# Kernel optimization log

Hardware: AMD Instinct MI355X
Metric: run time of the kernel (lower is better)

Reference implementation:

```python
import jax, jax.numpy as jnp
import numpy as np
import math

N_HEAD = 16
N_CTX = 1024


def setup_inputs() -> dict:
    key = jax.random.key(0)
    ks = jax.random.split(key, 3)
    B, S, NX = 4, 1024, 1024
    x = jax.random.normal(ks[0], (B, S, NX), dtype=jnp.float32)
    # Conv1D weights stored as [nx, nf], init std=0.02, bias zeros
    c_attn_w = jax.random.normal(ks[1], (NX, 3 * NX), dtype=jnp.float32) * 0.02
    c_attn_b = jnp.zeros((3 * NX,), dtype=jnp.float32)
    c_proj_w = jax.random.normal(ks[2], (NX, NX), dtype=jnp.float32) * 0.02
    c_proj_b = jnp.zeros((NX,), dtype=jnp.float32)
    return {"x": x, "c_attn_w": c_attn_w, "c_attn_b": c_attn_b,
            "c_proj_w": c_proj_w, "c_proj_b": c_proj_b}


def reference(x, c_attn_w, c_attn_b, c_proj_w, c_proj_b):
    B, S, NX = x.shape
    H = N_HEAD
    D = NX // H
    # c_attn: Conv1D -> x @ W + b, then split into q, k, v
    qkv = x @ c_attn_w + c_attn_b                      # [B,S,3*NX]
    q, k, v = jnp.split(qkv, 3, axis=-1)               # each [B,S,NX]
    # split heads: q,v -> [B,H,S,D]; k -> [B,H,D,S]
    q = q.reshape(B, S, H, D).transpose(0, 2, 1, 3)
    k = k.reshape(B, S, H, D).transpose(0, 2, 3, 1)
    v = v.reshape(B, S, H, D).transpose(0, 2, 1, 3)
    # _attn: scores, scale, combined multiplicative+additive causal mask, softmax
    w = jnp.matmul(q, k)                               # [B,H,S,S]
    w = w / math.sqrt(D)                               # scale=True
    bias = jnp.tril(jnp.ones((S, S), dtype=w.dtype))[None, None]  # causal tril slice
    w = w * bias - 1e10 * (1.0 - bias)
    w = jax.nn.softmax(w, axis=-1)
    a = jnp.matmul(w, v)                               # [B,H,S,D]
    # merge heads
    a = a.transpose(0, 2, 1, 3).reshape(B, S, NX)
    # c_proj
    return a @ c_proj_w + c_proj_b
```

## Files before the change

kernel.cpp:

```cpp
#include <hip/hip_runtime.h>
#include <cstdint>

typedef __attribute__((ext_vector_type(8))) short short8;
typedef __attribute__((ext_vector_type(4))) short short4x;
typedef __attribute__((ext_vector_type(4))) float floatx4;

__device__ __forceinline__ unsigned short f2b(float f) {
    unsigned int u = __builtin_bit_cast(unsigned int, f);
    u += 0x7fffu + ((u >> 16) & 1u);
    return (unsigned short)(u >> 16);
}
__device__ __forceinline__ float b2f(unsigned short s) {
    unsigned int u = ((unsigned int)s) << 16;
    return __builtin_bit_cast(float, u);
}
__device__ __forceinline__ float fast_exp2(float x) {
    float r;
    asm("v_exp_f32 %0, %1" : "=v"(r) : "v"(x));
    return r;
}
__device__ __forceinline__ unsigned int pack_bf16_trunc(float lo, float hi) {
    return __builtin_amdgcn_perm(__builtin_bit_cast(unsigned int, hi),
                                 __builtin_bit_cast(unsigned int, lo), 0x07060302u);
}

#define GLDS(g, l) __builtin_amdgcn_global_load_lds(                                   \
    (const __attribute__((address_space(1))) unsigned int*)(g),                        \
    (__attribute__((address_space(3))) unsigned int*)(l), 16, 0, 0)

__global__ __launch_bounds__(256) void prep_kernel(const float* __restrict__ x,
                                                   unsigned short* __restrict__ xb,
                                                   const float* __restrict__ w1,
                                                   unsigned short* __restrict__ w1t,
                                                   const float* __restrict__ w2,
                                                   unsigned short* __restrict__ w2t) {
    __shared__ unsigned short tile[64][65];
    const int b = blockIdx.x, t = threadIdx.x;
    if (b < 1024) {
        for (int i = b * 256 + t; i < 1048576; i += 262144) {
            float4 v = ((const float4*)x)[i];
            ushort4 o;
            o.x = f2b(v.x); o.y = f2b(v.y); o.z = f2b(v.z); o.w = f2b(v.w);
            ((ushort4*)xb)[i] = o;
        }
        return;
    }
    const float* W; unsigned short* Wt; int K, N, kb, nb;
    if (b < 1792) { W = w1; Wt = w1t; K = 1024; N = 3072; kb = (b - 1024) & 15; nb = (b - 1024) >> 4; }
    else          { W = w2; Wt = w2t; K = 1024; N = 1024; kb = (b - 1792) & 15; nb = (b - 1792) >> 4; }
    const int k0 = kb * 64, n0 = nb * 64;
    for (int idx = t; idx < 64 * 64; idx += 256) {
        int i = idx >> 6, j = idx & 63;
        tile[j][i] = f2b(W[(size_t)(k0 + i) * N + n0 + j]);
    }
    __syncthreads();
    for (int idx = t; idx < 64 * 64; idx += 256) {
        int r = idx >> 6, c = idx & 63;
        Wt[(size_t)(n0 + r) * K + k0 + c] = tile[r][c];
    }
}

__global__ __launch_bounds__(256) void gemm_bt_kernel(const unsigned short* __restrict__ A,
                                                      const unsigned short* __restrict__ Bt,
                                                      const float* __restrict__ bias,
                                                      unsigned short* __restrict__ C,
                                                      unsigned short* __restrict__ vTout,
                                                      int vSplit,
                                                      int M, int N, int K) {
    __shared__ unsigned short As[2][128][32];
    __shared__ unsigned short Bs[2][128][32];

    const int t = threadIdx.x;
    const int wave = t >> 6, lane = t & 63;
    const int quad = lane >> 4, l16 = lane & 15;
    const int rowBase = blockIdx.x * 128;
    const int colBase = blockIdx.y * 128;
    const int waveM = (wave >> 1) * 64;
    const int waveN = (wave & 1) * 64;

    floatx4 acc[4][4];
#pragma unroll
    for (int i = 0; i < 4; ++i)
#pragma unroll
        for (int j = 0; j < 4; ++j) acc[i][j] = (floatx4){0.f, 0.f, 0.f, 0.f};

    const int r0 = t >> 2, cc0 = (t & 3) * 8;
    const int r1 = 64 + (t >> 2);
    const unsigned short* aBase = A + (size_t)rowBase * K;
    const unsigned short* bBase = Bt + (size_t)colBase * K;

    auto stage = [&](int kk, int bf) {
        const int k0 = kk * 32;
        GLDS(aBase + (size_t)r0 * K + k0 + cc0, &As[bf][r0][cc0]);
        GLDS(aBase + (size_t)r1 * K + k0 + cc0, &As[bf][r1][cc0]);
        GLDS(bBase + (size_t)r0 * K + k0 + cc0, &Bs[bf][r0][cc0]);
        GLDS(bBase + (size_t)r1 * K + k0 + cc0, &Bs[bf][r1][cc0]);
    };

    const int nIter = K >> 5;
    stage(0, 0);

    for (int kk = 0; kk < nIter; ++kk) {
        __syncthreads();
        if (kk + 1 < nIter) stage(kk + 1, (kk + 1) & 1);
        const int buf = kk & 1;

        short8 af[4], bf[4];
#pragma unroll
        for (int mi = 0; mi < 4; ++mi)
            af[mi] = *(const short8*)&As[buf][waveM + mi * 16 + l16][quad * 8];
#pragma unroll
        for (int ni = 0; ni < 4; ++ni)
            bf[ni] = *(const short8*)&Bs[buf][waveN + ni * 16 + l16][quad * 8];
#pragma unroll
        for (int mi = 0; mi < 4; ++mi)
#pragma unroll
            for (int ni = 0; ni < 4; ++ni)
                acc[mi][ni] = __builtin_amdgcn_mfma_f32_16x16x32_bf16(af[mi], bf[ni], acc[mi][ni], 0, 0, 0);
    }

    if (colBase >= vSplit) {
#pragma unroll
        for (int mi = 0; mi < 4; ++mi)
#pragma unroll
            for (int ni = 0; ni < 4; ++ni) {
                int col = colBase + waveN + ni * 16 + l16 - vSplit;
                float bv = bias[colBase + waveN + ni * 16 + l16];
#pragma unroll
                for (int r = 0; r < 4; ++r) {
                    int row = rowBase + waveM + mi * 16 + quad * 4 + r;
                    vTout[((size_t)((row >> 10) * 16 + (col >> 6)) * 64 + (col & 63)) * 1024
                          + (row & 1023)] = f2b(acc[mi][ni][r] + bv);
                }
            }
    } else {
#pragma unroll
        for (int mi = 0; mi < 4; ++mi)
#pragma unroll
            for (int ni = 0; ni < 4; ++ni) {
                int col = colBase + waveN + ni * 16 + l16;
                float bv = bias[col];
#pragma unroll
                for (int r = 0; r < 4; ++r) {
                    int row = rowBase + waveM + mi * 16 + quad * 4 + r;
                    C[(size_t)row * N + col] = f2b(acc[mi][ni][r] + bv);
                }
            }
    }
}

__global__ __launch_bounds__(256) void gemm2_kernel(const unsigned short* __restrict__ A,
                                                    const unsigned short* __restrict__ Bt,
                                                    const float* __restrict__ bias,
                                                    float* __restrict__ C,
                                                    int M, int N, int K) {
    __shared__ unsigned short As[2][128][32];
    __shared__ unsigned short Bs[2][64][32];

    const int t = threadIdx.x;
    const int wave = t >> 6, lane = t & 63;
    const int quad = lane >> 4, l16 = lane & 15;
    const int rowBase = blockIdx.x * 128;
    const int colBase = blockIdx.y * 64;
    const int waveM = (wave >> 1) * 64;
    const int waveN = (wave & 1) * 32;

    floatx4 acc[4][2];
#pragma unroll
    for (int i = 0; i < 4; ++i)
#pragma unroll
        for (int j = 0; j < 2; ++j) acc[i][j] = (floatx4){0.f, 0.f, 0.f, 0.f};

    const int r0 = t >> 2, cc0 = (t & 3) * 8;
    const int r1 = 64 + (t >> 2);
    const unsigned short* aBase = A + (size_t)rowBase * K;
    const unsigned short* bBase = Bt + (size_t)colBase * K;

    auto stage = [&](int kk, int bf) {
        const int k0 = kk * 32;
        GLDS(aBase + (size_t)r0 * K + k0 + cc0, &As[bf][r0][cc0]);
        GLDS(aBase + (size_t)r1 * K + k0 + cc0, &As[bf][r1][cc0]);
        GLDS(bBase + (size_t)r0 * K + k0 + cc0, &Bs[bf][r0][cc0]);
    };

    const int nIter = K >> 5;
    stage(0, 0);

    for (int kk = 0; kk < nIter; ++kk) {
        __syncthreads();
        if (kk + 1 < nIter) stage(kk + 1, (kk + 1) & 1);
        const int buf = kk & 1;

        short8 af[4], bf[2];
#pragma unroll
        for (int mi = 0; mi < 4; ++mi)
            af[mi] = *(const short8*)&As[buf][waveM + mi * 16 + l16][quad * 8];
#pragma unroll
        for (int ni = 0; ni < 2; ++ni)
            bf[ni] = *(const short8*)&Bs[buf][waveN + ni * 16 + l16][quad * 8];
#pragma unroll
        for (int mi = 0; mi < 4; ++mi)
#pragma unroll
            for (int ni = 0; ni < 2; ++ni)
                acc[mi][ni] = __builtin_amdgcn_mfma_f32_16x16x32_bf16(af[mi], bf[ni], acc[mi][ni], 0, 0, 0);
    }

#pragma unroll
    for (int mi = 0; mi < 4; ++mi)
#pragma unroll
        for (int ni = 0; ni < 2; ++ni) {
            int col = colBase + waveN + ni * 16 + l16;
            float bv = bias[col];
#pragma unroll
            for (int r = 0; r < 4; ++r) {
                int row = rowBase + waveM + mi * 16 + quad * 4 + r;
                C[(size_t)row * N + col] = acc[mi][ni][r] + bv;
            }
        }
}

__global__ __launch_bounds__(256) void attn_kernel(const unsigned short* __restrict__ qkv,
                                                   const unsigned short* __restrict__ vT,
                                                   unsigned short* __restrict__ aout) {
    __shared__ unsigned short Ks[2][2][4096];
    __shared__ unsigned short Vs[2][2][4096];
    __shared__ unsigned short Tb[4][16 * 72];

    const int p  = blockIdx.x;
    const int bh = blockIdx.y;
    const int b = bh >> 4, h = bh & 15;
    const int qb1 = p, qb2 = 15 - p;
    const int t = threadIdx.x;
    const int wave = t >> 6, lane = t & 63;
    const int quad = lane >> 4, l16 = lane & 15;
    const int h7 = l16 & 7;

    const size_t rowB = (size_t)b * 1024;
    const size_t hoff = (size_t)h * 64;
    const int qA0 = qb1 * 64 + wave * 16;
    const int qB0 = qb2 * 64 + wave * 16;

    const float qscale = 0.125f * 1.44269504f;
    short8 qfA[2], qfB[2];
#pragma unroll
    for (int kc = 0; kc < 2; ++kc) {
        short8 qa = *(const short8*)(qkv + (rowB + qA0 + l16) * 3072 + hoff + kc * 32 + quad * 8);
        short8 qb = *(const short8*)(qkv + (rowB + qB0 + l16) * 3072 + hoff + kc * 32 + quad * 8);
#pragma unroll
        for (int e = 0; e < 8; ++e) {
            qa[e] = (short)f2b(b2f((unsigned short)qa[e]) * qscale);
            qb[e] = (short)f2b(b2f((unsigned short)qb[e]) * qscale);
        }
        qfA[kc] = qa; qfB[kc] = qb;
    }

    const int lr = lane >> 3;
    const int sc8 = (lane & 7) * 8;
    const int gc8 = ((lane & 7) ^ lr) * 8;
    const unsigned short* kSrc = qkv + rowB * 3072 + hoff + 1024;
    const unsigned short* vSrc = vT + (size_t)bh * 65536;

    auto stageT = [&](int kt, int bf, int sl) {
        const unsigned short* kp = kSrc + (size_t)kt * 64 * 3072;
        const unsigned short* vp = vSrc + kt * 64;
        int r0 = wave * 16 + lr, r1 = r0 + 8;
        GLDS(kp + (size_t)r0 * 3072 + gc8, &Ks[bf][sl][r0 * 64 + sc8]);
        GLDS(kp + (size_t)r1 * 3072 + gc8, &Ks[bf][sl][r1 * 64 + sc8]);
        GLDS(vp + (size_t)r0 * 1024 + gc8, &Vs[bf][sl][r0 * 64 + sc8]);
        GLDS(vp + (size_t)r1 * 1024 + gc8, &Vs[bf][sl][r1 * 64 + sc8]);
    };

    float lpA = 0.f, lpB = 0.f;
    floatx4 oA[4], oB[4];
#pragma unroll
    for (int ni = 0; ni < 4; ++ni) {
        oA[ni] = (floatx4){0.f, 0.f, 0.f, 0.f};
        oB[ni] = (floatx4){0.f, 0.f, 0.f, 0.f};
    }

    const int nT = qb2 + 1;
    const int nP = (nT + 1) >> 1;

    auto doTile = [&](int kt, const unsigned short* Kb, const unsigned short* Vb) {
        short8 kf[4][2];
#pragma unroll
        for (int jn = 0; jn < 4; ++jn)
#pragma unroll
            for (int kc = 0; kc < 2; ++kc)
                kf[jn][kc] = *(const short8*)&Kb[(jn * 16 + l16) * 64 + (((kc * 4 + quad) ^ h7) * 8)];
        short4x vf[4][4];
#pragma unroll
        for (int ni = 0; ni < 4; ++ni)
#pragma unroll
            for (int jb = 0; jb < 4; ++jb)
                vf[ni][jb] = *(const short4x*)&Vb[(ni * 16 + l16) * 64 +
                                                 (((jb * 2 + (quad >> 1)) ^ h7) * 8) + (quad & 1) * 4];

        auto qtile = [&](short8 (&qf)[2], floatx4 (&o)[4], float& lp, bool diag) {
            floatx4 s[4];
#pragma unroll
            for (int jn = 0; jn < 4; ++jn) s[jn] = (floatx4){0.f, 0.f, 0.f, 0.f};
#pragma unroll
            for (int jn = 0; jn < 4; ++jn)
#pragma unroll
                for (int kc = 0; kc < 2; ++kc)
                    s[jn] = __builtin_amdgcn_mfma_f32_16x16x32_bf16(kf[jn][kc], qf[kc], s[jn], 0, 0, 0);
            if (diag) {
                int ql = wave * 16 + l16;
#pragma unroll
                for (int jn = 0; jn < 4; ++jn)
#pragma unroll
                    for (int r = 0; r < 4; ++r)
                        if (jn * 16 + quad * 4 + r > ql) s[jn][r] = -1e30f;
            }
            short4x pb[4];
#pragma unroll
            for (int jb = 0; jb < 4; ++jb) {
                float pe0 = fast_exp2(s[jb][0]);
                float pe1 = fast_exp2(s[jb][1]);
                float pe2 = fast_exp2(s[jb][2]);
                float pe3 = fast_exp2(s[jb][3]);
                lp += (pe0 + pe1) + (pe2 + pe3);
                uint2 u;
                u.x = pack_bf16_trunc(pe0, pe1);
                u.y = pack_bf16_trunc(pe2, pe3);
                pb[jb] = __builtin_bit_cast(short4x, u);
            }
#pragma unroll
            for (int jb = 0; jb < 4; ++jb)
#pragma unroll
                for (int ni = 0; ni < 4; ++ni)
                    o[ni] = __builtin_amdgcn_mfma_f32_16x16x16bf16_1k(vf[ni][jb], pb[jb], o[ni], 0, 0, 0);
        };

        qtile(qfB, oB, lpB, kt == qb2);
        if (kt <= qb1) qtile(qfA, oA, lpA, kt == qb1);
    };

    stageT(0, 0, 0);
    stageT(1, 0, 1);

    for (int pi = 0; pi < nP; ++pi) {
        __syncthreads();
        if (pi + 1 < nP) {
            stageT(2 * pi + 2, (pi + 1) & 1, 0);
            if (2 * pi + 3 < nT) stageT(2 * pi + 3, (pi + 1) & 1, 1);
        }
        const int bfI = pi & 1;
        doTile(2 * pi, &Ks[bfI][0][0], &Vs[bfI][0][0]);
        if (2 * pi + 1 < nT) doTile(2 * pi + 1, &Ks[bfI][1][0], &Vs[bfI][1][0]);
    }

    lpA += __shfl_xor(lpA, 16); lpA += __shfl_xor(lpA, 32);
    lpB += __shfl_xor(lpB, 16); lpB += __shfl_xor(lpB, 32);
    const float liA = 1.f / lpA, liB = 1.f / lpB;

    auto writeOut = [&](floatx4 (&o)[4], float li, int q0) {
#pragma unroll
        for (int ni = 0; ni < 4; ++ni)
#pragma unroll
            for (int r = 0; r < 4; ++r)
                Tb[wave][l16 * 72 + ni * 16 + quad * 4 + r] = f2b(o[ni][r] * li);
#pragma unroll
        for (int i = 0; i < 2; ++i) {
            int q = lane >> 2, c = (lane & 3) + 4 * i;
            short8 v = *(const short8*)&Tb[wave][q * 72 + c * 8];
            *(short8*)(aout + (rowB + q0 + q) * 1024 + hoff + c * 8) = v;
        }
    };
    writeOut(oA, liA, qA0);
    writeOut(oB, liB, qB0);
}

extern "C" void kernel_launch(void* const* d_in, const int* in_sizes, int n_in,
                              void* d_out, int out_size, void* d_ws, size_t ws_size,
                              hipStream_t stream) {
    const float* x  = (const float*)d_in[0];
    const float* w1 = (const float*)d_in[1];
    const float* b1 = (const float*)d_in[2];
    const float* w2 = (const float*)d_in[3];
    const float* b2 = (const float*)d_in[4];
    float* out = (float*)d_out;

    unsigned short* xb   = (unsigned short*)d_ws;
    unsigned short* w1t  = xb  + (size_t)4096 * 1024;
    unsigned short* w2t  = w1t + (size_t)3072 * 1024;
    unsigned short* qkv  = w2t + (size_t)1024 * 1024;
    unsigned short* attn = qkv + (size_t)4096 * 3072;
    unsigned short* vTb  = attn + (size_t)4096 * 1024;

    prep_kernel<<<2048, 256, 0, stream>>>(x, xb, w1, w1t, w2, w2t);
    gemm_bt_kernel<<<dim3(32, 24), 256, 0, stream>>>(xb, w1t, b1, qkv, vTb, 2048,
                                                     4096, 3072, 1024);
    attn_kernel<<<dim3(8, 64), 256, 0, stream>>>(qkv, vTb, attn);
    gemm2_kernel<<<dim3(32, 16), 256, 0, stream>>>(attn, w2t, b2, out, 4096, 1024, 1024);
}
```

Before: 162.4 us.

## Rewrite QKV GEMM with 256x192 tiles, 8 waves, swizzled LDS and deeper prefetch

The QKV projection GEMM moves from 128x128 tiles with 4 waves to 256x192 tiles with 8 waves and a K-step of 64. LDS is XOR-swizzled to avoid bank conflicts, and global-to-LDS loads are staggered across phases with explicit vmcnt waits, barriers and setprio around the MFMA bursts, for roughly a two-stage prefetch. The grid becomes 16x16 = 256 blocks, about one per CU, to cut per-tile load overhead and raise MFMA utilisation. In exchange, K and N are hardcoded to 1024 and 3072, and the larger per-thread accumulator set raises register pressure.

```diff
diff --git a/kernel.cpp b/kernel.cpp
--- a/kernel.cpp
+++ b/kernel.cpp
@@ -60,92 +60,141 @@
     }
 }
 
-__global__ __launch_bounds__(256) void gemm_bt_kernel(const unsigned short* __restrict__ A,
-                                                      const unsigned short* __restrict__ Bt,
-                                                      const float* __restrict__ bias,
-                                                      unsigned short* __restrict__ C,
-                                                      unsigned short* __restrict__ vTout,
-                                                      int vSplit,
-                                                      int M, int N, int K) {
-    __shared__ unsigned short As[2][128][32];
-    __shared__ unsigned short Bs[2][128][32];
+#define MFMA16(a_, b_, c_) __builtin_amdgcn_mfma_f32_16x16x32_bf16((a_), (b_), (c_), 0, 0, 0)
+
+#define PH12(m0) do {                                              \
+    acc[(m0)][0]     = MFMA16(a00, b00, acc[(m0)][0]);             \
+    acc[(m0) + 1][0] = MFMA16(a10, b00, acc[(m0) + 1][0]);         \
+    acc[(m0)][1]     = MFMA16(a00, b10, acc[(m0)][1]);             \
+    acc[(m0) + 1][1] = MFMA16(a10, b10, acc[(m0) + 1][1]);         \
+    acc[(m0)][2]     = MFMA16(a00, b20, acc[(m0)][2]);             \
+    acc[(m0) + 1][2] = MFMA16(a10, b20, acc[(m0) + 1][2]);         \
+    acc[(m0)][0]     = MFMA16(a01, b01, acc[(m0)][0]);             \
+    acc[(m0) + 1][0] = MFMA16(a11, b01, acc[(m0) + 1][0]);         \
+    acc[(m0)][1]     = MFMA16(a01, b11, acc[(m0)][1]);             \
+    acc[(m0) + 1][1] = MFMA16(a11, b11, acc[(m0) + 1][1]);         \
+    acc[(m0)][2]     = MFMA16(a01, b21, acc[(m0)][2]);             \
+    acc[(m0) + 1][2] = MFMA16(a11, b21, acc[(m0) + 1][2]);         \
+} while (0)
+
+#define LDA(mi, kc) (*(const short8*)&As[buf][aRow + (mi) * 1024 + ((kc) ? g1 : g0)])
+#define LDB(ni, kc) (*(const short8*)&Bs[buf][bRow + (ni) * 1024 + ((kc) ? g1 : g0)])
+
+#define STAGE_A02(kt_) { const unsigned short* s_ = aSrc + (kt_) * 64;  \
+    GLDS(s_,             &As[(kt_) & 1][ldsOff]);                       \
+    GLDS(s_ + 128 * 1024, &As[(kt_) & 1][8192 + ldsOff]); }
+#define STAGE_A13(kt_) { const unsigned short* s_ = aSrc + (kt_) * 64;  \
+    GLDS(s_ + 64 * 1024,  &As[(kt_) & 1][4096 + ldsOff]);               \
+    GLDS(s_ + 192 * 1024, &As[(kt_) & 1][12288 + ldsOff]); }
+#define STAGE_B3(kt_) { const unsigned short* s_ = bSrc + (kt_) * 64;   \
+    GLDS(s_,             &Bs[(kt_) & 1][ldsOff]);                       \
+    GLDS(s_ + 64 * 1024,  &Bs[(kt_) & 1][4096 + ldsOff]);               \
+    GLDS(s_ + 128 * 1024, &Bs[(kt_) & 1][8192 + ldsOff]); }
+
+__global__ __launch_bounds__(512, 2) void gemm_bt_kernel(const unsigned short* __restrict__ A,
+                                                         const unsigned short* __restrict__ Bt,
+                                                         const float* __restrict__ bias,
+                                                         unsigned short* __restrict__ C,
+                                                         unsigned short* __restrict__ vTout,
+                                                         int vSplit) {
+    __shared__ unsigned short As[2][256 * 64];
+    __shared__ unsigned short Bs[2][192 * 64];
 
     const int t = threadIdx.x;
     const int wave = t >> 6, lane = t & 63;
     const int quad = lane >> 4, l16 = lane & 15;
-    const int rowBase = blockIdx.x * 128;
-    const int colBase = blockIdx.y * 128;
-    const int waveM = (wave >> 1) * 64;
-    const int waveN = (wave & 1) * 64;
-
-    floatx4 acc[4][4];
-#pragma unroll
-    for (int i = 0; i < 4; ++i)
-#pragma unroll
-        for (int j = 0; j < 4; ++j) acc[i][j] = (floatx4){0.f, 0.f, 0.f, 0.f};
-
-    const int r0 = t >> 2, cc0 = (t & 3) * 8;
-    const int r1 = 64 + (t >> 2);
-    const unsigned short* aBase = A + (size_t)rowBase * K;
-    const unsigned short* bBase = Bt + (size_t)colBase * K;
-
-    auto stage = [&](int kk, int bf) {
-        const int k0 = kk * 32;
-        GLDS(aBase + (size_t)r0 * K + k0 + cc0, &As[bf][r0][cc0]);
-        GLDS(aBase + (size_t)r1 * K + k0 + cc0, &As[bf][r1][cc0]);
-        GLDS(bBase + (size_t)r0 * K + k0 + cc0, &Bs[bf][r0][cc0]);
-        GLDS(bBase + (size_t)r1 * K + k0 + cc0, &Bs[bf][r1][cc0]);
-    };
-
-    const int nIter = K >> 5;
-    stage(0, 0);
-
-    for (int kk = 0; kk < nIter; ++kk) {
-        __syncthreads();
-        if (kk + 1 < nIter) stage(kk + 1, (kk + 1) & 1);
-        const int buf = kk & 1;
-
-        short8 af[4], bf[4];
-#pragma unroll
-        for (int mi = 0; mi < 4; ++mi)
-            af[mi] = *(const short8*)&As[buf][waveM + mi * 16 + l16][quad * 8];
-#pragma unroll
-        for (int ni = 0; ni < 4; ++ni)
-            bf[ni] = *(const short8*)&Bs[buf][waveN + ni * 16 + l16][quad * 8];
-#pragma unroll
-        for (int mi = 0; mi < 4; ++mi)
-#pragma unroll
-            for (int ni = 0; ni < 4; ++ni)
-                acc[mi][ni] = __builtin_amdgcn_mfma_f32_16x16x32_bf16(af[mi], bf[ni], acc[mi][ni], 0, 0, 0);
-    }
-
-    if (colBase >= vSplit) {
-#pragma unroll
-        for (int mi = 0; mi < 4; ++mi)
-#pragma unroll
-            for (int ni = 0; ni < 4; ++ni) {
-                int col = colBase + waveN + ni * 16 + l16 - vSplit;
-                float bv = bias[colBase + waveN + ni * 16 + l16];
+    const int wm = wave >> 2, wn = wave & 3;
+    const int rowBase = blockIdx.x << 8;
+    const int colBase = blockIdx.y * 192;
+
+    floatx4 acc[8][3];
+#pragma unroll
+    for (int i = 0; i < 8; ++i)
+#pragma unroll
+        for (int j = 0; j < 3; ++j) acc[i][j] = (floatx4){0.f, 0.f, 0.f, 0.f};
+
+    const int rr = t >> 3;
+    const int gsrc = ((t & 7) ^ (rr & 7)) * 8;
+    const unsigned short* aSrc = A + (size_t)(rowBase + rr) * 1024 + gsrc;
+    const unsigned short* bSrc = Bt + (size_t)(colBase + rr) * 1024 + gsrc;
+    const int ldsOff = t * 8;
+
+    const int rg = l16 & 7;
+    const int g0 = (quad ^ rg) * 8;
+    const int g1 = g0 ^ 32;
+    const int aRow = (wm * 128 + l16) * 64;
+    const int bRow = (wn * 48 + l16) * 64;
+
+    STAGE_B3(0); STAGE_A02(0); STAGE_A13(0); STAGE_B3(1); STAGE_A02(1);
+    asm volatile("s_waitcnt vmcnt(7)" ::: "memory");
+    __builtin_amdgcn_s_barrier();
+
+    for (int kt = 0; kt < 14; ++kt) {
+        const int buf = kt & 1;
+        short8 b00, b01, b10, b11, b20, b21;
+#pragma unroll
+        for (int p = 0; p < 4; ++p) {
+            if (p == 0) {
+                b00 = LDB(0, 0); b01 = LDB(0, 1);
+                b10 = LDB(1, 0); b11 = LDB(1, 1);
+                b20 = LDB(2, 0); b21 = LDB(2, 1);
+            }
+            short8 a00 = LDA(2 * p, 0),     a01 = LDA(2 * p, 1);
+            short8 a10 = LDA(2 * p + 1, 0), a11 = LDA(2 * p + 1, 1);
+            if (p == 0) STAGE_A13(kt + 1);
+            if (p == 1) STAGE_B3(kt + 2);
+            if (p == 2) STAGE_A02(kt + 2);
+            if (p == 1) asm volatile("s_waitcnt vmcnt(10)" ::: "memory");
+            if (p == 3) asm volatile("s_waitcnt vmcnt(7)" ::: "memory");
+            __builtin_amdgcn_s_barrier();
+            asm volatile("s_waitcnt lgkmcnt(0)" ::: "memory");
+            __builtin_amdgcn_s_setprio(1);
+            PH12(2 * p);
+            __builtin_amdgcn_s_setprio(0);
+            __builtin_amdgcn_s_barrier();
+        }
+    }
+
+    STAGE_A13(15);
+    asm volatile("s_waitcnt vmcnt(0)" ::: "memory");
+    __builtin_amdgcn_s_barrier();
+#pragma unroll
+    for (int kt2 = 14; kt2 < 16; ++kt2) {
+        const int buf = kt2 & 1;
+        short8 b00 = LDB(0, 0), b01 = LDB(0, 1);
+        short8 b10 = LDB(1, 0), b11 = LDB(1, 1);
+        short8 b20 = LDB(2, 0), b21 = LDB(2, 1);
+#pragma unroll
+        for (int m0 = 0; m0 < 8; m0 += 2) {
+            short8 a00 = LDA(m0, 0),     a01 = LDA(m0, 1);
+            short8 a10 = LDA(m0 + 1, 0), a11 = LDA(m0 + 1, 1);
+            PH12(m0);
+        }
+    }
+
+#pragma unroll
+    for (int mi = 0; mi < 8; ++mi) {
+        const int row0 = rowBase + wm * 128 + mi * 16 + quad * 4;
+#pragma unroll
+        for (int ni = 0; ni < 3; ++ni) {
+            const int colA = colBase + wn * 48 + ni * 16 + l16;
+            const float bv = bias[colA];
+            if (colA >= vSplit) {
+                const int vcol = colA - vSplit;
 #pragma unroll
                 for (int r = 0; r < 4; ++r) {
-                    int row = rowBase + waveM + mi * 16 + quad * 4 + r;
-                    vTout[((size_t)((row >> 10) * 16 + (col >> 6)) * 64 + (col & 63)) * 1024
+                    const int row = row0 + r;
+                    vTout[((size_t)((row >> 10) * 16 + (vcol >> 6)) * 64 + (vcol & 63)) * 1024
                           + (row & 1023)] = f2b(acc[mi][ni][r] + bv);
                 }
-            }
-    } else {
-#pragma unroll
-        for (int mi = 0; mi < 4; ++mi)
-#pragma unroll
-            for (int ni = 0; ni < 4; ++ni) {
-                int col = colBase + waveN + ni * 16 + l16;
-                float bv = bias[col];
+            } else {
 #pragma unroll
                 for (int r = 0; r < 4; ++r) {
-                    int row = rowBase + waveM + mi * 16 + quad * 4 + r;
-                    C[(size_t)row * N + col] = f2b(acc[mi][ni][r] + bv);
+                    const int row = row0 + r;
+                    C[(size_t)row * 3072 + colA] = f2b(acc[mi][ni][r] + bv);
                 }
             }
+        }
     }
 }
 
@@ -390,8 +439,7 @@
     unsigned short* vTb  = attn + (size_t)4096 * 1024;
 
     prep_kernel<<<2048, 256, 0, stream>>>(x, xb, w1, w1t, w2, w2t);
-    gemm_bt_kernel<<<dim3(32, 24), 256, 0, stream>>>(xb, w1t, b1, qkv, vTb, 2048,
-                                                     4096, 3072, 1024);
+    gemm_bt_kernel<<<dim3(16, 16), 512, 0, stream>>>(xb, w1t, b1, qkv, vTb, 2048);
     attn_kernel<<<dim3(8, 64), 256, 0, stream>>>(qkv, vTb, attn);
     gemm2_kernel<<<dim3(32, 16), 256, 0, stream>>>(attn, w2t, b2, out, 4096, 1024, 1024);
 }
```

Measured after the change: 168.6 us. 3.8% more time.

## Shrink QKV GEMM tile to 128x64, swizzle block order, vectorize V-transpose stores

Applied to the files above, without the earlier changes.

The QKV projection GEMM now uses 128x64 output tiles, doubling the grid from 768 to 1536 blocks for better occupancy and load balance across CUs. A block-index swizzle groups blocks so that neighbouring blocks reuse A/B tiles in L2. The transposed-V epilogue packs four bf16 values into one 8-byte store instead of four 2-byte scattered stores. Dimensions are hardcoded as constants. The cost is lower arithmetic intensity per block and more total global loads of the A matrix.

```diff
diff --git a/kernel.cpp b/kernel.cpp
--- a/kernel.cpp
+++ b/kernel.cpp
@@ -60,90 +60,97 @@
     }
 }
 
+#define MFMA16(a_, b_, c_) __builtin_amdgcn_mfma_f32_16x16x32_bf16((a_), (b_), (c_), 0, 0, 0)
+
 __global__ __launch_bounds__(256) void gemm_bt_kernel(const unsigned short* __restrict__ A,
                                                       const unsigned short* __restrict__ Bt,
                                                       const float* __restrict__ bias,
                                                       unsigned short* __restrict__ C,
                                                       unsigned short* __restrict__ vTout,
-                                                      int vSplit,
-                                                      int M, int N, int K) {
+                                                      int vSplit) {
     __shared__ unsigned short As[2][128][32];
-    __shared__ unsigned short Bs[2][128][32];
+    __shared__ unsigned short Bs[2][64][32];
 
     const int t = threadIdx.x;
     const int wave = t >> 6, lane = t & 63;
     const int quad = lane >> 4, l16 = lane & 15;
-    const int rowBase = blockIdx.x * 128;
-    const int colBase = blockIdx.y * 128;
+    const int flat = blockIdx.y * 32 + blockIdx.x;
+    const int swz = (flat & 7) * 192 + (flat >> 3);
+    const int rowBase = (swz & 31) << 7;
+    const int colBase = (swz >> 5) << 6;
     const int waveM = (wave >> 1) * 64;
-    const int waveN = (wave & 1) * 64;
-
-    floatx4 acc[4][4];
+    const int waveN = (wave & 1) * 32;
+
+    floatx4 acc[4][2];
 #pragma unroll
     for (int i = 0; i < 4; ++i)
 #pragma unroll
-        for (int j = 0; j < 4; ++j) acc[i][j] = (floatx4){0.f, 0.f, 0.f, 0.f};
+        for (int j = 0; j < 2; ++j) acc[i][j] = (floatx4){0.f, 0.f, 0.f, 0.f};
 
     const int r0 = t >> 2, cc0 = (t & 3) * 8;
     const int r1 = 64 + (t >> 2);
-    const unsigned short* aBase = A + (size_t)rowBase * K;
-    const unsigned short* bBase = Bt + (size_t)colBase * K;
+    const unsigned short* aBase = A + (size_t)rowBase * 1024;
+    const unsigned short* bBase = Bt + (size_t)colBase * 1024;
 
     auto stage = [&](int kk, int bf) {
         const int k0 = kk * 32;
-        GLDS(aBase + (size_t)r0 * K + k0 + cc0, &As[bf][r0][cc0]);
-        GLDS(aBase + (size_t)r1 * K + k0 + cc0, &As[bf][r1][cc0]);
-        GLDS(bBase + (size_t)r0 * K + k0 + cc0, &Bs[bf][r0][cc0]);
-        GLDS(bBase + (size_t)r1 * K + k0 + cc0, &Bs[bf][r1][cc0]);
+        GLDS(aBase + (size_t)r0 * 1024 + k0 + cc0, &As[bf][r0][cc0]);
+        GLDS(aBase + (size_t)r1 * 1024 + k0 + cc0, &As[bf][r1][cc0]);
+        GLDS(bBase + (size_t)r0 * 1024 + k0 + cc0, &Bs[bf][r0][cc0]);
     };
 
-    const int nIter = K >> 5;
     stage(0, 0);
 
-    for (int kk = 0; kk < nIter; ++kk) {
+    for (int kk = 0; kk < 32; ++kk) {
         __syncthreads();
-        if (kk + 1 < nIter) stage(kk + 1, (kk + 1) & 1);
+        if (kk + 1 < 32) stage(kk + 1, (kk + 1) & 1);
         const int buf = kk & 1;
 
-        short8 af[4], bf[4];
+        short8 af[4], bf[2];
 #pragma unroll
         for (int mi = 0; mi < 4; ++mi)
             af[mi] = *(const short8*)&As[buf][waveM + mi * 16 + l16][quad * 8];
 #pragma unroll
-        for (int ni = 0; ni < 4; ++ni)
+        for (int ni = 0; ni < 2; ++ni)
             bf[ni] = *(const short8*)&Bs[buf][waveN + ni * 16 + l16][quad * 8];
 #pragma unroll
         for (int mi = 0; mi < 4; ++mi)
 #pragma unroll
-            for (int ni = 0; ni < 4; ++ni)
-                acc[mi][ni] = __builtin_amdgcn_mfma_f32_16x16x32_bf16(af[mi], bf[ni], acc[mi][ni], 0, 0, 0);
+            for (int ni = 0; ni < 2; ++ni)
+                acc[mi][ni] = MFMA16(af[mi], bf[ni], acc[mi][ni]);
     }
 
     if (colBase >= vSplit) {
 #pragma unroll
         for (int mi = 0; mi < 4; ++mi)
 #pragma unroll
-            for (int ni = 0; ni < 4; ++ni) {
-                int col = colBase + waveN + ni * 16 + l16 - vSplit;
-                float bv = bias[colBase + waveN + ni * 16 + l16];
+            for (int ni = 0; ni < 2; ++ni) {
+                int colq = colBase + waveN + ni * 16 + l16;
+                int col = colq - vSplit;
+                float bv = bias[colq];
+                int row0 = rowBase + waveM + mi * 16 + quad * 4;
+                unsigned short e0 = f2b(acc[mi][ni][0] + bv);
+                unsigned short e1 = f2b(acc[mi][ni][1] + bv);
+                unsigned short e2 = f2b(acc[mi][ni][2] + bv);
+                unsigned short e3 = f2b(acc[mi][ni][3] + bv);
+                uint2 uu;
+                uu.x = (unsigned int)e0 | ((unsigned int)e1 << 16);
+                uu.y = (unsigned int)e2 | ((unsigned int)e3 << 16);
+                size_t idx = ((size_t)((row0 >> 10) * 16 + (col >> 6)) * 64 + (col & 63)) * 1024
+                             + (row0 & 1023);
+                *(uint2*)&vTout[idx] = uu;
+            }
+    } else {
+#pragma unroll
+        for (int mi = 0; mi < 4; ++mi)
+#pragma unroll
+            for (int ni = 0; ni < 2; ++ni) {
+                int col = colBase + waveN + ni * 16 + l16;
+                float bv = bias[col];
 #pragma unroll
                 for (int r = 0; r < 4; ++r) {
                     int row = rowBase + waveM + mi * 16 + quad * 4 + r;
-                    vTout[((size_t)((row >> 10) * 16 + (col >> 6)) * 64 + (col & 63)) * 1024
-                          + (row & 1023)] = f2b(acc[mi][ni][r] + bv);
-                }
-            }
-    } else {
-#pragma unroll
-        for (int mi = 0; mi < 4; ++mi)
-#pragma unroll
-            for (int ni = 0; ni < 4; ++ni) {
-                int col = colBase + waveN + ni * 16 + l16;
-                float bv = bias[col];
-#pragma unroll
-                for (int r = 0; r < 4; ++r) {
-                    int row = rowBase + waveM + mi * 16 + quad * 4 + r;
-                    C[(size_t)row * N + col] = f2b(acc[mi][ni][r] + bv);
+                    C[(size_t)row * 3072 + col] = f2b(acc[mi][ni][r] + bv);
                 }
             }
     }
@@ -202,7 +209,7 @@
         for (int mi = 0; mi < 4; ++mi)
 #pragma unroll
             for (int ni = 0; ni < 2; ++ni)
-                acc[mi][ni] = __builtin_amdgcn_mfma_f32_16x16x32_bf16(af[mi], bf[ni], acc[mi][ni], 0, 0, 0);
+                acc[mi][ni] = MFMA16(af[mi], bf[ni], acc[mi][ni]);
     }
 
 #pragma unroll
@@ -390,8 +397,7 @@
     unsigned short* vTb  = attn + (size_t)4096 * 1024;
 
     prep_kernel<<<2048, 256, 0, stream>>>(x, xb, w1, w1t, w2, w2t);
-    gemm_bt_kernel<<<dim3(32, 24), 256, 0, stream>>>(xb, w1t, b1, qkv, vTb, 2048,
-                                                     4096, 3072, 1024);
+    gemm_bt_kernel<<<dim3(32, 48), 256, 0, stream>>>(xb, w1t, b1, qkv, vTb, 2048);
     attn_kernel<<<dim3(8, 64), 256, 0, stream>>>(qkv, vTb, attn);
     gemm2_kernel<<<dim3(32, 16), 256, 0, stream>>>(attn, w2t, b2, out, 4096, 1024, 1024);
 }
```

After: 180.6 us. 1.11x slower.
